# Kernel optimization log

Hardware: AMD Instinct MI355X
Metric: run time of the kernel (lower is better)

The kernel has to match this reference:

```python
import jax, jax.numpy as jnp
import numpy as np

INPUT_SIZE = 2048
HIDDEN_SIZE = 2048
BATCH = 4096


def setup_inputs() -> dict:
    key = jax.random.key(0)
    ks = jax.random.split(key, 12)
    D = INPUT_SIZE + HIDDEN_SIZE
    H = HIDDEN_SIZE
    s = 1.0 / np.sqrt(D)  # torch nn.Linear default init scale
    def lin(k):
        kw, kb = jax.random.split(k)
        W = jax.random.uniform(kw, (H, D), jnp.float32, -s, s)
        b = jax.random.uniform(kb, (H,), jnp.float32, -s, s)
        return W, b
    W_i, b_i = lin(ks[0])
    W_f, b_f = lin(ks[1])
    W_o, b_o = lin(ks[2])
    W_c, b_c = lin(ks[3])
    x_t = jax.random.normal(ks[4], (BATCH, INPUT_SIZE), jnp.float32)
    h_t_1 = jax.random.normal(ks[5], (BATCH, HIDDEN_SIZE), jnp.float32)
    c_t_1 = jax.random.normal(ks[6], (BATCH, HIDDEN_SIZE), jnp.float32)
    return {
        "x_t": x_t, "h_t_1": h_t_1, "c_t_1": c_t_1,
        "W_i": W_i, "b_i": b_i,
        "W_f": W_f, "b_f": b_f,
        "W_o": W_o, "b_o": b_o,
        "W_c": W_c, "b_c": b_c,
    }


def reference(x_t, h_t_1, c_t_1, W_i, b_i, W_f, b_f, W_o, b_o, W_c, b_c):
    # xh: [B, input_size + hidden_size]
    xh = jnp.concatenate([x_t, h_t_1], axis=1)
    # Fuse the 4 independent gate GEMMs into one matmul with stacked weights.
    W = jnp.concatenate([W_i, W_f, W_o, W_c], axis=0)  # [4H, D]
    b = jnp.concatenate([b_i, b_f, b_o, b_c], axis=0)  # [4H]
    z = xh @ W.T + b  # [B, 4H]
    H = W_i.shape[0]
    zi, zf, zo, zc = jnp.split(z, 4, axis=1)
    i_t = jax.nn.sigmoid(zi)
    f_t = jax.nn.sigmoid(zf)
    o_t = jax.nn.sigmoid(zo)
    c_hat = jnp.tanh(zc)
    c_t = f_t * c_t_1 + i_t * c_hat
    h_t = o_t * jnp.tanh(c_t)
    return (h_t, c_t)
```

## Files before the change

### kernel.cpp

```cpp
#include <hip/hip_runtime.h>
#include <hip/hip_bf16.h>


#define M_DIM 4096
#define K_DIM 4096
#define H_DIM 2048
#define BM 256
#define BH 32
#define BK 64
#define NTHREADS 512

typedef __attribute__((ext_vector_type(8))) short bf16x8;
typedef __attribute__((ext_vector_type(8))) unsigned short u16x8;
typedef __attribute__((ext_vector_type(4))) float f32x4;

__device__ __forceinline__ unsigned short f2bf(float f) {
    union { float f; unsigned int u; } v; v.f = f;
    unsigned int u = v.u;
    unsigned int r = u + 0x7FFFu + ((u >> 16) & 1u);
    return (unsigned short)(r >> 16);
}

__device__ __forceinline__ float sigmoid_f(float x) {
    return 1.0f / (1.0f + __expf(-x));
}
__device__ __forceinline__ float tanh_f(float x) {
    return 2.0f / (1.0f + __expf(-2.0f * x)) - 1.0f;
}

__device__ __forceinline__ int sw64(int row, int koff) {
    int c  = koff >> 3;
    int sc = c ^ (row & 7);
    return row * BK + sc * 8 + (koff & 7);
}

__device__ __forceinline__ void async_load16(const unsigned short* g, unsigned short* l) {
    __builtin_amdgcn_global_load_lds(
        (const __attribute__((address_space(1))) void*)g,
        (__attribute__((address_space(3))) void*)l,
        16, 0, 0);
}

__global__ __launch_bounds__(256) void convert_all(
        const float* __restrict__ x, const float* __restrict__ h,
        const float* __restrict__ Wi, const float* __restrict__ Wf,
        const float* __restrict__ Wo, const float* __restrict__ Wc,
        u16x8* __restrict__ xh_bf, u16x8* __restrict__ w_bf) {
    const int XHT = (M_DIM * K_DIM) / 8;
    int t = blockIdx.x * 256 + threadIdx.x;
    const float* src;
    u16x8* dst;
    if (t < XHT) {
        int e = t * 8;
        int row = e >> 12;
        int col = e & 4095;
        src = (col < 2048) ? &x[(size_t)row * 2048 + col]
                           : &h[(size_t)row * 2048 + (col - 2048)];
        dst = xh_bf + t;
    } else {
        int g2 = t - XHT;
        long e = (long)g2 * 8;
        int row = (int)(e >> 12);
        int col = (int)(e & 4095);
        int gate = row >> 11;
        const float* Ws = (gate == 0) ? Wi : (gate == 1) ? Wf : (gate == 2) ? Wo : Wc;
        src = &Ws[(size_t)(row & 2047) * 4096 + col];
        dst = w_bf + g2;
    }
    float4 v0 = *(const float4*)src;
    float4 v1 = *(const float4*)(src + 4);
    u16x8 o;
    o[0] = f2bf(v0.x); o[1] = f2bf(v0.y); o[2] = f2bf(v0.z); o[3] = f2bf(v0.w);
    o[4] = f2bf(v1.x); o[5] = f2bf(v1.y); o[6] = f2bf(v1.z); o[7] = f2bf(v1.w);
    *dst = o;
}

template <bool DMA>
__global__ __launch_bounds__(NTHREADS, 2) void lstm_gemm(
    const unsigned short* __restrict__ xh_bf, const unsigned short* __restrict__ w_bf,
    const float* __restrict__ x_t, const float* __restrict__ h_t_1,
    const float* __restrict__ Wi, const float* __restrict__ Wf,
    const float* __restrict__ Wo, const float* __restrict__ Wc,
    const float* __restrict__ b_i, const float* __restrict__ b_f,
    const float* __restrict__ b_o, const float* __restrict__ b_c,
    const float* __restrict__ c_prev,
    float* __restrict__ h_out, float* __restrict__ c_out) {

    __shared__ __align__(16) unsigned short sA[BM * BK];
    __shared__ __align__(16) unsigned short sB[4 * BH * BK];

    const int tid  = threadIdx.x;
    const int w    = tid >> 6;
    const int lane = tid & 63;
    const int l16  = lane & 15;
    const int quad = lane >> 4;
    const int wm   = w & 3;
    const int wh   = w >> 2;
    const int s7   = l16 & 7;

    const int bid  = blockIdx.x;
    const int xcd  = bid & 7;
    const int slot = bid >> 3;
    const int yIdx = xcd * 2 + (slot >> 6);
    const int nIdx = slot & 63;

    const int mBase = yIdx * BM;
    const int nBase = nIdx * BH;

    f32x4 acc[4][4] = {};

    const int aBase = (wm * 64 + l16) * BK;
    const int bBase = (wh * 16 + l16) * BK;

    const unsigned short* aSrc = nullptr;
    const unsigned short* bSrc = nullptr;
    if constexpr (DMA) {
        int arowi = tid >> 3;
        int alc   = (tid & 7) ^ (arowi & 7);
        aSrc = xh_bf + (size_t)(mBase + arowi) * K_DIM + alc * 8;
        int browi = (tid >> 3) & 31;
        int gate0 = tid >> 8;
        int blc   = (tid & 7) ^ (browi & 7);
        bSrc = w_bf + (size_t)(gate0 * H_DIM + nBase + browi) * K_DIM + blc * 8;
    }
    const int dmaDst = tid * 8;

    for (int k0 = 0; k0 < K_DIM; k0 += BK) {
        __syncthreads();
        if constexpr (DMA) {
#pragma unroll
            for (int r = 0; r < 4; ++r)
                async_load16(aSrc + (size_t)r * 64 * K_DIM, &sA[dmaDst + r * 4096]);
#pragma unroll
            for (int r = 0; r < 2; ++r)
                async_load16(bSrc + (size_t)r * 2 * H_DIM * K_DIM, &sB[dmaDst + r * 4096]);
            aSrc += BK;
            bSrc += BK;
        } else {
            const float* Asrc = (k0 < 2048) ? x_t : h_t_1;
            int kloc = k0 & 2047;
#pragma unroll
            for (int r = 0; r < 8; ++r) {
                int cc  = r * NTHREADS + tid;
                int row = cc >> 4;
                int ko  = (cc & 15) * 4;
                float4 v = *(const float4*)&Asrc[(size_t)(mBase + row) * 2048 + kloc + ko];
                *(ushort4*)&sA[sw64(row, ko)] =
                    make_ushort4(f2bf(v.x), f2bf(v.y), f2bf(v.z), f2bf(v.w));
            }
            const float* Wg[4] = {Wi, Wf, Wo, Wc};
#pragma unroll
            for (int r = 0; r < 4; ++r) {
                int cc   = r * NTHREADS + tid;
                int gate = cc >> 9;
                int row  = (cc >> 4) & 31;
                int ko   = (cc & 15) * 4;
                float4 v = *(const float4*)&Wg[gate][(size_t)(nBase + row) * K_DIM + k0 + ko];
                *(ushort4*)&sB[gate * (BH * BK) + sw64(row, ko)] =
                    make_ushort4(f2bf(v.x), f2bf(v.y), f2bf(v.z), f2bf(v.w));
            }
        }
        __syncthreads();

#pragma unroll
        for (int hk = 0; hk < 2; ++hk) {
            const int co = ((hk * 4 + quad) ^ s7) << 3;
            bf16x8 av[4];
#pragma unroll
            for (int mt = 0; mt < 4; ++mt)
                av[mt] = *(const bf16x8*)&sA[aBase + mt * (16 * BK) + co];
            bf16x8 bv[4];
#pragma unroll
            for (int g = 0; g < 4; ++g)
                bv[g] = *(const bf16x8*)&sB[g * (BH * BK) + bBase + co];
#pragma unroll
            for (int g = 0; g < 4; ++g)
#pragma unroll
                for (int mt = 0; mt < 4; ++mt)
                    acc[g][mt] = __builtin_amdgcn_mfma_f32_16x16x32_bf16(
                        av[mt], bv[g], acc[g][mt], 0, 0, 0);
        }
    }

    {
        int n = nBase + wh * 16 + l16;
        float bi = b_i[n], bf = b_f[n], bo = b_o[n], bc = b_c[n];
#pragma unroll
        for (int mt = 0; mt < 4; ++mt) {
#pragma unroll
            for (int i = 0; i < 4; ++i) {
                int m = mBase + wm * 64 + mt * 16 + quad * 4 + i;
                float zi = acc[0][mt][i] + bi;
                float zf = acc[1][mt][i] + bf;
                float zo = acc[2][mt][i] + bo;
                float zc = acc[3][mt][i] + bc;
                float ig = sigmoid_f(zi);
                float fg = sigmoid_f(zf);
                float og = sigmoid_f(zo);
                float ch = tanh_f(zc);
                size_t idx = (size_t)m * H_DIM + n;
                float c = fg * c_prev[idx] + ig * ch;
                c_out[idx] = c;
                h_out[idx] = og * tanh_f(c);
            }
        }
    }
}

extern "C" void kernel_launch(void* const* d_in, const int* in_sizes, int n_in,
                              void* d_out, int out_size, void* d_ws, size_t ws_size,
                              hipStream_t stream) {
    const float* x_t   = (const float*)d_in[0];
    const float* h_t_1 = (const float*)d_in[1];
    const float* c_t_1 = (const float*)d_in[2];
    const float* W_i   = (const float*)d_in[3];
    const float* b_i   = (const float*)d_in[4];
    const float* W_f   = (const float*)d_in[5];
    const float* b_f   = (const float*)d_in[6];
    const float* W_o   = (const float*)d_in[7];
    const float* b_o   = (const float*)d_in[8];
    const float* W_c   = (const float*)d_in[9];
    const float* b_c   = (const float*)d_in[10];

    float* h_out = (float*)d_out;
    float* c_out = h_out + (size_t)M_DIM * H_DIM;

    dim3 grid((H_DIM / BH) * (M_DIM / BM));

    const size_t need = (size_t)M_DIM * K_DIM * 2 + (size_t)4 * H_DIM * K_DIM * 2;
    if (ws_size >= need) {
        unsigned short* xh_bf = (unsigned short*)d_ws;
        unsigned short* w_bf  = xh_bf + (size_t)M_DIM * K_DIM;
        int total_threads = (M_DIM * K_DIM + 4 * H_DIM * K_DIM) / 8;
        convert_all<<<total_threads / 256, 256, 0, stream>>>(
            x_t, h_t_1, W_i, W_f, W_o, W_c, (u16x8*)xh_bf, (u16x8*)w_bf);
        lstm_gemm<true><<<grid, NTHREADS, 0, stream>>>(
            xh_bf, w_bf, nullptr, nullptr, nullptr, nullptr, nullptr, nullptr,
            b_i, b_f, b_o, b_c, c_t_1, h_out, c_out);
    } else {
        lstm_gemm<false><<<grid, NTHREADS, 0, stream>>>(
            nullptr, nullptr, x_t, h_t_1, W_i, W_f, W_o, W_c,
            b_i, b_f, b_o, b_c, c_t_1, h_out, c_out);
    }
}
```

Measured before the change: 519.3 us.

## Add double-buffered, larger-tile GEMM kernel with XCD-aware block mapping

Adds a new LSTM GEMM kernel that double-buffers the A and B tiles in LDS, issuing async loads for the next K-step between MFMA phases. The tile grows from 32 to 64 hidden columns per gate, and s_setprio raises wave priority around the MFMA phases. Blocks are remapped so that each XCD handles contiguous M rows, which should improve L2 reuse. The aim is to hide global-load latency and raise arithmetic intensity, at the cost of twice the LDS and more accumulator registers (128 floats per thread), which may reduce occupancy.

```diff
diff --git a/kernel.cpp b/kernel.cpp
--- a/kernel.cpp
+++ b/kernel.cpp
@@ -5,10 +5,16 @@
 #define M_DIM 4096
 #define K_DIM 4096
 #define H_DIM 2048
+#define BK 64
+
 #define BM 256
 #define BH 32
-#define BK 64
 #define NTHREADS 512
+
+#define BM2 256
+#define BH2 64
+#define NT2 512
+#define KT (K_DIM / BK)
 
 typedef __attribute__((ext_vector_type(8))) short bf16x8;
 typedef __attribute__((ext_vector_type(8))) unsigned short u16x8;
@@ -75,6 +81,165 @@
     *dst = o;
 }
 
+__global__ __launch_bounds__(NT2, 2) void lstm_gemm_pipe(
+    const unsigned short* __restrict__ xh_bf, const unsigned short* __restrict__ w_bf,
+    const float* __restrict__ b_i, const float* __restrict__ b_f,
+    const float* __restrict__ b_o, const float* __restrict__ b_c,
+    const float* __restrict__ c_prev,
+    float* __restrict__ h_out, float* __restrict__ c_out) {
+
+    __shared__ __align__(16) unsigned short sA2[2][BM2 * BK];
+    __shared__ __align__(16) unsigned short sB2[2][4 * BH2 * BK];
+
+    const int tid  = threadIdx.x;
+    const int w    = tid >> 6;
+    const int lane = tid & 63;
+    const int l16  = lane & 15;
+    const int quad = lane >> 4;
+    const int wm   = w >> 2;
+    const int wh   = w & 3;
+    const int s7   = l16 & 7;
+
+    const int bid  = blockIdx.x;
+    const int xcd  = bid & 7;
+    const int slot = bid >> 3;
+    const int mRow = xcd * 2 + (slot >> 5);
+    const int nIdx = slot & 31;
+    const int mBase = mRow * BM2;
+    const int nBase = nIdx * BH2;
+
+    f32x4 acc[4][8] = {};
+
+    const int r0  = tid >> 3;
+    const int c8  = ((tid & 7) ^ (r0 & 7)) << 3;
+    const unsigned short* aS = xh_bf + (size_t)(mBase + r0) * K_DIM + c8;
+    const int g0  = (r0 >> 4) & 3;
+    const int hr0 = r0 & 15;
+    const unsigned short* bS = w_bf + (size_t)(g0 * H_DIM + nBase + hr0) * K_DIM + c8;
+    const int dstA = tid * 8;
+
+#pragma unroll
+    for (int r = 0; r < 4; ++r)
+        async_load16(aS + (size_t)r * 64 * K_DIM, &sA2[0][dstA + r * 4096]);
+#pragma unroll
+    for (int r = 0; r < 4; ++r)
+        async_load16(bS + (size_t)r * 16 * K_DIM, &sB2[0][dstA + r * 4096]);
+    __syncthreads();
+
+    const int aO0 = (wm * 128 + l16) * BK;
+    const int bO0 = (wh * 64 + l16) * BK;
+    const int co0 = (quad ^ s7) << 3;
+    const int co1 = ((4 + quad) ^ s7) << 3;
+
+    for (int t = 0; t < KT; ++t) {
+        const unsigned short* sAb = sA2[t & 1];
+        const unsigned short* sBb = sB2[t & 1];
+        unsigned short* dA = sA2[(t + 1) & 1];
+        unsigned short* dB = sB2[(t + 1) & 1];
+        const unsigned short* aN = aS + (size_t)(t + 1) * BK;
+        const unsigned short* bN = bS + (size_t)(t + 1) * BK;
+        const bool st = (t + 1 < KT);
+
+        bf16x8 av[4], bv[4];
+
+#pragma unroll
+        for (int mt = 0; mt < 4; ++mt)
+            av[mt] = *(const bf16x8*)&sAb[aO0 + co0 + mt * (16 * BK)];
+#pragma unroll
+        for (int g = 0; g < 4; ++g)
+            bv[g] = *(const bf16x8*)&sBb[bO0 + co0 + g * (16 * BK)];
+        if (st) {
+#pragma unroll
+            for (int r = 0; r < 4; ++r)
+                async_load16(aN + (size_t)r * 64 * K_DIM, &dA[dstA + r * 4096]);
+        }
+        __builtin_amdgcn_s_barrier();
+        __builtin_amdgcn_s_setprio(1);
+#pragma unroll
+        for (int g = 0; g < 4; ++g)
+#pragma unroll
+            for (int mt = 0; mt < 4; ++mt)
+                acc[g][mt] = __builtin_amdgcn_mfma_f32_16x16x32_bf16(
+                    av[mt], bv[g], acc[g][mt], 0, 0, 0);
+        __builtin_amdgcn_s_setprio(0);
+        __builtin_amdgcn_s_barrier();
+
+#pragma unroll
+        for (int mt = 0; mt < 4; ++mt)
+            av[mt] = *(const bf16x8*)&sAb[aO0 + co0 + (mt + 4) * (16 * BK)];
+        if (st) {
+#pragma unroll
+            for (int r = 0; r < 4; ++r)
+                async_load16(bN + (size_t)r * 16 * K_DIM, &dB[dstA + r * 4096]);
+        }
+        __builtin_amdgcn_s_barrier();
+        __builtin_amdgcn_s_setprio(1);
+#pragma unroll
+        for (int g = 0; g < 4; ++g)
+#pragma unroll
+            for (int mt = 0; mt < 4; ++mt)
+                acc[g][mt + 4] = __builtin_amdgcn_mfma_f32_16x16x32_bf16(
+                    av[mt], bv[g], acc[g][mt + 4], 0, 0, 0);
+        __builtin_amdgcn_s_setprio(0);
+        __builtin_amdgcn_s_barrier();
+
+#pragma unroll
+        for (int mt = 0; mt < 4; ++mt)
+            av[mt] = *(const bf16x8*)&sAb[aO0 + co1 + mt * (16 * BK)];
+#pragma unroll
+        for (int g = 0; g < 4; ++g)
+            bv[g] = *(const bf16x8*)&sBb[bO0 + co1 + g * (16 * BK)];
+        __builtin_amdgcn_s_barrier();
+        __builtin_amdgcn_s_setprio(1);
+#pragma unroll
+        for (int g = 0; g < 4; ++g)
+#pragma unroll
+            for (int mt = 0; mt < 4; ++mt)
+                acc[g][mt] = __builtin_amdgcn_mfma_f32_16x16x32_bf16(
+                    av[mt], bv[g], acc[g][mt], 0, 0, 0);
+        __builtin_amdgcn_s_setprio(0);
+        __builtin_amdgcn_s_barrier();
+
+#pragma unroll
+        for (int mt = 0; mt < 4; ++mt)
+            av[mt] = *(const bf16x8*)&sAb[aO0 + co1 + (mt + 4) * (16 * BK)];
+        __builtin_amdgcn_s_barrier();
+        __builtin_amdgcn_s_setprio(1);
+#pragma unroll
+        for (int g = 0; g < 4; ++g)
+#pragma unroll
+            for (int mt = 0; mt < 4; ++mt)
+                acc[g][mt + 4] = __builtin_amdgcn_mfma_f32_16x16x32_bf16(
+                    av[mt], bv[g], acc[g][mt + 4], 0, 0, 0);
+        __builtin_amdgcn_s_setprio(0);
+        __syncthreads();
+    }
+
+    {
+        const int n = nBase + wh * 16 + l16;
+        const float bi = b_i[n], bff = b_f[n], bo = b_o[n], bc = b_c[n];
+#pragma unroll
+        for (int mt = 0; mt < 8; ++mt) {
+#pragma unroll
+            for (int i = 0; i < 4; ++i) {
+                int m = mBase + wm * 128 + mt * 16 + quad * 4 + i;
+                float zi = acc[0][mt][i] + bi;
+                float zf = acc[1][mt][i] + bff;
+                float zo = acc[2][mt][i] + bo;
+                float zc = acc[3][mt][i] + bc;
+                float ig = sigmoid_f(zi);
+                float fg = sigmoid_f(zf);
+                float og = sigmoid_f(zo);
+                float ch = tanh_f(zc);
+                size_t idx = (size_t)m * H_DIM + n;
+                float c = fg * c_prev[idx] + ig * ch;
+                c_out[idx] = c;
+                h_out[idx] = og * tanh_f(c);
+            }
+        }
+    }
+}
+
 template <bool DMA>
 __global__ __launch_bounds__(NTHREADS, 2) void lstm_gemm(
     const unsigned short* __restrict__ xh_bf, const unsigned short* __restrict__ w_bf,
@@ -225,8 +390,6 @@
     float* h_out = (float*)d_out;
     float* c_out = h_out + (size_t)M_DIM * H_DIM;
 
-    dim3 grid((H_DIM / BH) * (M_DIM / BM));
-
     const size_t need = (size_t)M_DIM * K_DIM * 2 + (size_t)4 * H_DIM * K_DIM * 2;
     if (ws_size >= need) {
         unsigned short* xh_bf = (unsigned short*)d_ws;
@@ -234,10 +397,11 @@
         int total_threads = (M_DIM * K_DIM + 4 * H_DIM * K_DIM) / 8;
         convert_all<<<total_threads / 256, 256, 0, stream>>>(
             x_t, h_t_1, W_i, W_f, W_o, W_c, (u16x8*)xh_bf, (u16x8*)w_bf);
-        lstm_gemm<true><<<grid, NTHREADS, 0, stream>>>(
-            xh_bf, w_bf, nullptr, nullptr, nullptr, nullptr, nullptr, nullptr,
-            b_i, b_f, b_o, b_c, c_t_1, h_out, c_out);
+        dim3 grid((H_DIM / BH2) * (M_DIM / BM2));
+        lstm_gemm_pipe<<<grid, NT2, 0, stream>>>(
+            xh_bf, w_bf, b_i, b_f, b_o, b_c, c_t_1, h_out, c_out);
     } else {
+        dim3 grid((H_DIM / BH) * (M_DIM / BM));
         lstm_gemm<false><<<grid, NTHREADS, 0, stream>>>(
             nullptr, nullptr, x_t, h_t_1, W_i, W_f, W_o, W_c,
             b_i, b_f, b_o, b_c, c_t_1, h_out, c_out);
```

New measurement: 566.5 us. +9.1%, slower.

## Add 4-stage async-load pipelined GEMM with larger N tile and split barriers

Applied to the files above, without the earlier changes.

Replaces the single-buffered DMA GEMM with a new kernel that keeps four shared-memory stages and issues async loads three tiles ahead, so global loads overlap MFMA work instead of waiting behind a full barrier each K step. The tile grows to 256x64 (per gate 64 hidden columns), giving each wave 32 accumulators and halving the grid. K is split into 32-wide steps, and s_setprio and barriers interleave LDS reads, DMA issue and MFMA. This needs more LDS and registers, which may cut occupancy, and depends on hand-tuned vmcnt waits being correct.

```diff
diff --git a/kernel.cpp b/kernel.cpp
--- a/kernel.cpp
+++ b/kernel.cpp
@@ -5,10 +5,18 @@
 #define M_DIM 4096
 #define K_DIM 4096
 #define H_DIM 2048
+
 #define BM 256
 #define BH 32
 #define BK 64
 #define NTHREADS 512
+
+#define BM2 256
+#define BH2 64
+#define BKP 32
+#define NT2 512
+#define KT2 (K_DIM / BKP)
+#define TILE_SH (BM2 * BKP)
 
 typedef __attribute__((ext_vector_type(8))) short bf16x8;
 typedef __attribute__((ext_vector_type(8))) unsigned short u16x8;
@@ -75,9 +83,149 @@
     *dst = o;
 }
 
-template <bool DMA>
-__global__ __launch_bounds__(NTHREADS, 2) void lstm_gemm(
+
+#define TILE_STEP(T, DO_STG, WAIT_OP) do {                                        \
+    const int cur_ = (T) & 3;                                                     \
+    const unsigned short* sAc = &sA[cur_ * TILE_SH];                              \
+    const unsigned short* sBc = &sB[cur_ * TILE_SH];                              \
+                            \
+    bf16x8 av0_[4], bv_[4];                                                       \
+    _Pragma("unroll")                                                             \
+    for (int mt = 0; mt < 4; ++mt)                                                \
+        av0_[mt] = *(const bf16x8*)&sAc[aOff + mt * (16 * BKP)];                  \
+    _Pragma("unroll")                                                             \
+    for (int g = 0; g < 4; ++g)                                                   \
+        bv_[g] = *(const bf16x8*)&sBc[bOff + g * (16 * BKP)];                     \
+    if (DO_STG) {                                                                 \
+        unsigned short* dA = &sA[(((T) + 3) & 3) * TILE_SH];                      \
+        const unsigned short* s0 = aS + (size_t)((T) + 3) * BKP;                  \
+        async_load16(s0, &dA[dstOff]);                                            \
+        async_load16(s0 + (size_t)128 * K_DIM, &dA[dstOff + 4096]);               \
+    }                                                                             \
+    __builtin_amdgcn_s_barrier();                                                 \
+    __builtin_amdgcn_s_setprio(1);                                                \
+    _Pragma("unroll")                                                             \
+    for (int g = 0; g < 4; ++g)                                                   \
+        _Pragma("unroll")                                                         \
+        for (int mt = 0; mt < 4; ++mt)                                            \
+            acc[g][mt] = __builtin_amdgcn_mfma_f32_16x16x32_bf16(                 \
+                av0_[mt], bv_[g], acc[g][mt], 0, 0, 0);                           \
+    __builtin_amdgcn_s_setprio(0);                                                \
+    __builtin_amdgcn_s_barrier();                                                 \
+                \
+    bf16x8 av1_[4];                                                               \
+    _Pragma("unroll")                                                             \
+    for (int mt = 0; mt < 4; ++mt)                                                \
+        av1_[mt] = *(const bf16x8*)&sAc[aOff + (mt + 4) * (16 * BKP)];            \
+    if (DO_STG) {                                                                 \
+        unsigned short* dB = &sB[(((T) + 3) & 3) * TILE_SH];                      \
+        const unsigned short* s1 = bS + (size_t)((T) + 3) * BKP;                  \
+        async_load16(s1, &dB[dstOff]);                                            \
+        async_load16(s1 + (size_t)32 * K_DIM, &dB[dstOff + 4096]);                \
+    }                                                                             \
+    __builtin_amdgcn_s_barrier();                                                 \
+    __builtin_amdgcn_s_setprio(1);                                                \
+    _Pragma("unroll")                                                             \
+    for (int g = 0; g < 4; ++g)                                                   \
+        _Pragma("unroll")                                                         \
+        for (int mt = 0; mt < 4; ++mt)                                            \
+            acc[g][mt + 4] = __builtin_amdgcn_mfma_f32_16x16x32_bf16(             \
+                av1_[mt], bv_[g], acc[g][mt + 4], 0, 0, 0);                       \
+    __builtin_amdgcn_s_setprio(0);                                                \
+    WAIT_OP;                                                                      \
+    __builtin_amdgcn_s_barrier();                                                 \
+} while (0)
+
+__global__ __launch_bounds__(NT2, 2) void lstm_gemm_pipe(
     const unsigned short* __restrict__ xh_bf, const unsigned short* __restrict__ w_bf,
+    const float* __restrict__ b_i, const float* __restrict__ b_f,
+    const float* __restrict__ b_o, const float* __restrict__ b_c,
+    const float* __restrict__ c_prev,
+    float* __restrict__ h_out, float* __restrict__ c_out) {
+
+    __shared__ __align__(16) unsigned short sA[4 * TILE_SH];
+    __shared__ __align__(16) unsigned short sB[4 * TILE_SH];
+
+    const int tid  = threadIdx.x;
+    const int w    = tid >> 6;
+    const int lane = tid & 63;
+    const int l16  = lane & 15;
+    const int quad = lane >> 4;
+    const int wm   = w >> 2;
+    const int wh   = w & 3;
+
+    const int bid  = blockIdx.x;
+    const int xcd  = bid & 7;
+    const int slot = bid >> 3;
+    const int mRow = xcd * 2 + (slot >> 5);
+    const int nIdx = slot & 31;
+    const int mBase = mRow * BM2;
+    const int nBase = nIdx * BH2;
+
+    f32x4 acc[4][8] = {};
+
+    const int c8a  = (((tid & 3) ^ ((tid >> 3) & 3)) << 3);
+    const int row0 = tid >> 2;
+    const unsigned short* aS = xh_bf + (size_t)(mBase + row0) * K_DIM + c8a;
+    const int q0   = row0 >> 6;
+    const int gat0 = (row0 >> 4) & 3;
+    const int hr0  = row0 & 15;
+    const unsigned short* bS =
+        w_bf + (size_t)(gat0 * H_DIM + nBase + q0 * 16 + hr0) * K_DIM + c8a;
+    const int dstOff = tid * 8;
+
+    const int slotSh = ((quad ^ ((l16 >> 1) & 3)) << 3);
+    const int aOff = (wm * 128 + l16) * BKP + slotSh;
+    const int bOff = (wh * 64 + l16) * BKP + slotSh;
+
+#pragma unroll
+    for (int p = 0; p < 3; ++p) {
+        const unsigned short* a0 = aS + (size_t)p * BKP;
+        const unsigned short* b0 = bS + (size_t)p * BKP;
+        unsigned short* dA = &sA[p * TILE_SH];
+        unsigned short* dB = &sB[p * TILE_SH];
+        async_load16(a0, &dA[dstOff]);
+        async_load16(a0 + (size_t)128 * K_DIM, &dA[dstOff + 4096]);
+        async_load16(b0, &dB[dstOff]);
+        async_load16(b0 + (size_t)32 * K_DIM, &dB[dstOff + 4096]);
+    }
+    asm volatile("s_waitcnt vmcnt(8)" ::: "memory");
+    __builtin_amdgcn_s_barrier();
+
+#pragma unroll 1
+    for (int t = 0; t < KT2 - 3; ++t) {
+        TILE_STEP(t, true, asm volatile("s_waitcnt vmcnt(8)" ::: "memory"));
+    }
+    TILE_STEP(KT2 - 3, false, asm volatile("s_waitcnt vmcnt(4)" ::: "memory"));
+    TILE_STEP(KT2 - 2, false, asm volatile("s_waitcnt vmcnt(0)" ::: "memory"));
+    TILE_STEP(KT2 - 1, false, (void)0);
+
+    {
+        const int n = nBase + wh * 16 + l16;
+        const float bi = b_i[n], bff = b_f[n], bo = b_o[n], bc = b_c[n];
+#pragma unroll
+        for (int mt = 0; mt < 8; ++mt) {
+#pragma unroll
+            for (int i = 0; i < 4; ++i) {
+                int m = mBase + wm * 128 + mt * 16 + quad * 4 + i;
+                float zi = acc[0][mt][i] + bi;
+                float zf = acc[1][mt][i] + bff;
+                float zo = acc[2][mt][i] + bo;
+                float zc = acc[3][mt][i] + bc;
+                float ig = sigmoid_f(zi);
+                float fg = sigmoid_f(zf);
+                float og = sigmoid_f(zo);
+                float ch = tanh_f(zc);
+                size_t idx = (size_t)m * H_DIM + n;
+                float c = fg * c_prev[idx] + ig * ch;
+                c_out[idx] = c;
+                h_out[idx] = og * tanh_f(c);
+            }
+        }
+    }
+}
+
+__global__ __launch_bounds__(NTHREADS, 2) void lstm_gemm_fb(
     const float* __restrict__ x_t, const float* __restrict__ h_t_1,
     const float* __restrict__ Wi, const float* __restrict__ Wf,
     const float* __restrict__ Wo, const float* __restrict__ Wc,
@@ -112,53 +260,29 @@
     const int aBase = (wm * 64 + l16) * BK;
     const int bBase = (wh * 16 + l16) * BK;
 
-    const unsigned short* aSrc = nullptr;
-    const unsigned short* bSrc = nullptr;
-    if constexpr (DMA) {
-        int arowi = tid >> 3;
-        int alc   = (tid & 7) ^ (arowi & 7);
-        aSrc = xh_bf + (size_t)(mBase + arowi) * K_DIM + alc * 8;
-        int browi = (tid >> 3) & 31;
-        int gate0 = tid >> 8;
-        int blc   = (tid & 7) ^ (browi & 7);
-        bSrc = w_bf + (size_t)(gate0 * H_DIM + nBase + browi) * K_DIM + blc * 8;
-    }
-    const int dmaDst = tid * 8;
-
     for (int k0 = 0; k0 < K_DIM; k0 += BK) {
         __syncthreads();
-        if constexpr (DMA) {
-#pragma unroll
-            for (int r = 0; r < 4; ++r)
-                async_load16(aSrc + (size_t)r * 64 * K_DIM, &sA[dmaDst + r * 4096]);
-#pragma unroll
-            for (int r = 0; r < 2; ++r)
-                async_load16(bSrc + (size_t)r * 2 * H_DIM * K_DIM, &sB[dmaDst + r * 4096]);
-            aSrc += BK;
-            bSrc += BK;
-        } else {
-            const float* Asrc = (k0 < 2048) ? x_t : h_t_1;
-            int kloc = k0 & 2047;
-#pragma unroll
-            for (int r = 0; r < 8; ++r) {
-                int cc  = r * NTHREADS + tid;
-                int row = cc >> 4;
-                int ko  = (cc & 15) * 4;
-                float4 v = *(const float4*)&Asrc[(size_t)(mBase + row) * 2048 + kloc + ko];
-                *(ushort4*)&sA[sw64(row, ko)] =
-                    make_ushort4(f2bf(v.x), f2bf(v.y), f2bf(v.z), f2bf(v.w));
-            }
-            const float* Wg[4] = {Wi, Wf, Wo, Wc};
-#pragma unroll
-            for (int r = 0; r < 4; ++r) {
-                int cc   = r * NTHREADS + tid;
-                int gate = cc >> 9;
-                int row  = (cc >> 4) & 31;
-                int ko   = (cc & 15) * 4;
-                float4 v = *(const float4*)&Wg[gate][(size_t)(nBase + row) * K_DIM + k0 + ko];
-                *(ushort4*)&sB[gate * (BH * BK) + sw64(row, ko)] =
-                    make_ushort4(f2bf(v.x), f2bf(v.y), f2bf(v.z), f2bf(v.w));
-            }
+        const float* Asrc = (k0 < 2048) ? x_t : h_t_1;
+        int kloc = k0 & 2047;
+#pragma unroll
+        for (int r = 0; r < 8; ++r) {
+            int cc  = r * NTHREADS + tid;
+            int row = cc >> 4;
+            int ko  = (cc & 15) * 4;
+            float4 v = *(const float4*)&Asrc[(size_t)(mBase + row) * 2048 + kloc + ko];
+            *(ushort4*)&sA[sw64(row, ko)] =
+                make_ushort4(f2bf(v.x), f2bf(v.y), f2bf(v.z), f2bf(v.w));
+        }
+        const float* Wg[4] = {Wi, Wf, Wo, Wc};
+#pragma unroll
+        for (int r = 0; r < 4; ++r) {
+            int cc   = r * NTHREADS + tid;
+            int gate = cc >> 9;
+            int row  = (cc >> 4) & 31;
+            int ko   = (cc & 15) * 4;
+            float4 v = *(const float4*)&Wg[gate][(size_t)(nBase + row) * K_DIM + k0 + ko];
+            *(ushort4*)&sB[gate * (BH * BK) + sw64(row, ko)] =
+                make_ushort4(f2bf(v.x), f2bf(v.y), f2bf(v.z), f2bf(v.w));
         }
         __syncthreads();
 
@@ -225,8 +349,6 @@
     float* h_out = (float*)d_out;
     float* c_out = h_out + (size_t)M_DIM * H_DIM;
 
-    dim3 grid((H_DIM / BH) * (M_DIM / BM));
-
     const size_t need = (size_t)M_DIM * K_DIM * 2 + (size_t)4 * H_DIM * K_DIM * 2;
     if (ws_size >= need) {
         unsigned short* xh_bf = (unsigned short*)d_ws;
@@ -234,12 +356,13 @@
         int total_threads = (M_DIM * K_DIM + 4 * H_DIM * K_DIM) / 8;
         convert_all<<<total_threads / 256, 256, 0, stream>>>(
             x_t, h_t_1, W_i, W_f, W_o, W_c, (u16x8*)xh_bf, (u16x8*)w_bf);
-        lstm_gemm<true><<<grid, NTHREADS, 0, stream>>>(
-            xh_bf, w_bf, nullptr, nullptr, nullptr, nullptr, nullptr, nullptr,
+        dim3 grid((H_DIM / BH2) * (M_DIM / BM2));
+        lstm_gemm_pipe<<<grid, NT2, 0, stream>>>(
+            xh_bf, w_bf, b_i, b_f, b_o, b_c, c_t_1, h_out, c_out);
+    } else {
+        dim3 grid((H_DIM / BH) * (M_DIM / BM));
+        lstm_gemm_fb<<<grid, NTHREADS, 0, stream>>>(
+            x_t, h_t_1, W_i, W_f, W_o, W_c,
             b_i, b_f, b_o, b_c, c_t_1, h_out, c_out);
-    } else {
-        lstm_gemm<false><<<grid, NTHREADS, 0, stream>>>(
-            nullptr, nullptr, x_t, h_t_1, W_i, W_f, W_o, W_c,
-            b_i, b_f, b_o, b_c, c_t_1, h_out, c_out);
-    }
-}
+    }
+}
```

New measurement: 565.6 us. 8.9% more time.

## Double-buffer A tile in LDS and load weight fragments directly into registers

Applied to the files above, without the earlier changes.

The DMA GEMM path now double-buffers the activation tile in shared memory, issuing the next tile's async loads before computing on the current one, and drops one barrier per K step. Weight fragments are read straight from global memory into registers instead of being staged through LDS. Launch bounds rise to 4 blocks per SM and MFMA sections are wrapped in s_setprio. This aims to hide global load latency and cut LDS traffic, but direct per-lane weight reads rely on cache hits, and higher occupancy may limit registers.

```diff
diff --git a/kernel.cpp b/kernel.cpp
--- a/kernel.cpp
+++ b/kernel.cpp
@@ -75,19 +75,14 @@
     *dst = o;
 }
 
-template <bool DMA>
-__global__ __launch_bounds__(NTHREADS, 2) void lstm_gemm(
+__global__ __launch_bounds__(NTHREADS, 4) void lstm_gemm_dbv(
     const unsigned short* __restrict__ xh_bf, const unsigned short* __restrict__ w_bf,
-    const float* __restrict__ x_t, const float* __restrict__ h_t_1,
-    const float* __restrict__ Wi, const float* __restrict__ Wf,
-    const float* __restrict__ Wo, const float* __restrict__ Wc,
     const float* __restrict__ b_i, const float* __restrict__ b_f,
     const float* __restrict__ b_o, const float* __restrict__ b_c,
     const float* __restrict__ c_prev,
     float* __restrict__ h_out, float* __restrict__ c_out) {
 
-    __shared__ __align__(16) unsigned short sA[BM * BK];
-    __shared__ __align__(16) unsigned short sB[4 * BH * BK];
+    __shared__ __align__(16) unsigned short sA[2][BM * BK];
 
     const int tid  = threadIdx.x;
     const int w    = tid >> 6;
@@ -109,56 +104,159 @@
 
     f32x4 acc[4][4] = {};
 
+    const int arowi = tid >> 3;
+    const int alc   = (tid & 7) ^ (arowi & 7);
+    const unsigned short* aS = xh_bf + (size_t)(mBase + arowi) * K_DIM + alc * 8;
+    const int dmaDst = tid * 8;
+
+    const unsigned short* bvBase =
+        w_bf + (size_t)(nBase + wh * 16 + l16) * K_DIM + quad * 8;
+
+    const int aBase = (wm * 64 + l16) * BK;
+
+#pragma unroll
+    for (int r = 0; r < 4; ++r)
+        async_load16(aS + (size_t)r * 64 * K_DIM, &sA[0][dmaDst + r * 4096]);
+    __syncthreads();
+
+#pragma unroll 1
+    for (int t = 0; t < K_DIM / BK; ++t) {
+        const unsigned short* sAc = sA[t & 1];
+        unsigned short* sAn = (unsigned short*)sA[(t + 1) & 1];
+        const int k0 = t * BK;
+
+        if (t < (K_DIM / BK) - 1) {
+            const unsigned short* an = aS + (size_t)(k0 + BK);
+#pragma unroll
+            for (int r = 0; r < 4; ++r)
+                async_load16(an + (size_t)r * 64 * K_DIM, &sAn[dmaDst + r * 4096]);
+        }
+
+        bf16x8 bv0[4], bv1[4];
+#pragma unroll
+        for (int g = 0; g < 4; ++g)
+            bv0[g] = *(const bf16x8*)(bvBase + (size_t)g * H_DIM * K_DIM + k0);
+#pragma unroll
+        for (int g = 0; g < 4; ++g)
+            bv1[g] = *(const bf16x8*)(bvBase + (size_t)g * H_DIM * K_DIM + k0 + 32);
+
+        {
+            const int co = (quad ^ s7) << 3;
+            bf16x8 av[4];
+#pragma unroll
+            for (int mt = 0; mt < 4; ++mt)
+                av[mt] = *(const bf16x8*)&sAc[aBase + mt * (16 * BK) + co];
+            __builtin_amdgcn_s_setprio(1);
+#pragma unroll
+            for (int g = 0; g < 4; ++g)
+#pragma unroll
+                for (int mt = 0; mt < 4; ++mt)
+                    acc[g][mt] = __builtin_amdgcn_mfma_f32_16x16x32_bf16(
+                        av[mt], bv0[g], acc[g][mt], 0, 0, 0);
+            __builtin_amdgcn_s_setprio(0);
+        }
+        {
+            const int co = ((4 + quad) ^ s7) << 3;
+            bf16x8 av[4];
+#pragma unroll
+            for (int mt = 0; mt < 4; ++mt)
+                av[mt] = *(const bf16x8*)&sAc[aBase + mt * (16 * BK) + co];
+            __builtin_amdgcn_s_setprio(1);
+#pragma unroll
+            for (int g = 0; g < 4; ++g)
+#pragma unroll
+                for (int mt = 0; mt < 4; ++mt)
+                    acc[g][mt] = __builtin_amdgcn_mfma_f32_16x16x32_bf16(
+                        av[mt], bv1[g], acc[g][mt], 0, 0, 0);
+            __builtin_amdgcn_s_setprio(0);
+        }
+
+        __syncthreads();
+    }
+
+    {
+        const int n = nBase + wh * 16 + l16;
+        const float bi = b_i[n], bff = b_f[n], bo = b_o[n], bc = b_c[n];
+#pragma unroll
+        for (int mt = 0; mt < 4; ++mt) {
+#pragma unroll
+            for (int i = 0; i < 4; ++i) {
+                int m = mBase + wm * 64 + mt * 16 + quad * 4 + i;
+                float zi = acc[0][mt][i] + bi;
+                float zf = acc[1][mt][i] + bff;
+                float zo = acc[2][mt][i] + bo;
+                float zc = acc[3][mt][i] + bc;
+                float ig = sigmoid_f(zi);
+                float fg = sigmoid_f(zf);
+                float og = sigmoid_f(zo);
+                float ch = tanh_f(zc);
+                size_t idx = (size_t)m * H_DIM + n;
+                float c = fg * c_prev[idx] + ig * ch;
+                c_out[idx] = c;
+                h_out[idx] = og * tanh_f(c);
+            }
+        }
+    }
+}
+
+__global__ __launch_bounds__(NTHREADS, 2) void lstm_gemm_fb(
+    const float* __restrict__ x_t, const float* __restrict__ h_t_1,
+    const float* __restrict__ Wi, const float* __restrict__ Wf,
+    const float* __restrict__ Wo, const float* __restrict__ Wc,
+    const float* __restrict__ b_i, const float* __restrict__ b_f,
+    const float* __restrict__ b_o, const float* __restrict__ b_c,
+    const float* __restrict__ c_prev,
+    float* __restrict__ h_out, float* __restrict__ c_out) {
+
+    __shared__ __align__(16) unsigned short sA[BM * BK];
+    __shared__ __align__(16) unsigned short sB[4 * BH * BK];
+
+    const int tid  = threadIdx.x;
+    const int w    = tid >> 6;
+    const int lane = tid & 63;
+    const int l16  = lane & 15;
+    const int quad = lane >> 4;
+    const int wm   = w & 3;
+    const int wh   = w >> 2;
+    const int s7   = l16 & 7;
+
+    const int bid  = blockIdx.x;
+    const int xcd  = bid & 7;
+    const int slot = bid >> 3;
+    const int yIdx = xcd * 2 + (slot >> 6);
+    const int nIdx = slot & 63;
+
+    const int mBase = yIdx * BM;
+    const int nBase = nIdx * BH;
+
+    f32x4 acc[4][4] = {};
+
     const int aBase = (wm * 64 + l16) * BK;
     const int bBase = (wh * 16 + l16) * BK;
 
-    const unsigned short* aSrc = nullptr;
-    const unsigned short* bSrc = nullptr;
-    if constexpr (DMA) {
-        int arowi = tid >> 3;
-        int alc   = (tid & 7) ^ (arowi & 7);
-        aSrc = xh_bf + (size_t)(mBase + arowi) * K_DIM + alc * 8;
-        int browi = (tid >> 3) & 31;
-        int gate0 = tid >> 8;
-        int blc   = (tid & 7) ^ (browi & 7);
-        bSrc = w_bf + (size_t)(gate0 * H_DIM + nBase + browi) * K_DIM + blc * 8;
-    }
-    const int dmaDst = tid * 8;
-
     for (int k0 = 0; k0 < K_DIM; k0 += BK) {
         __syncthreads();
-        if constexpr (DMA) {
-#pragma unroll
-            for (int r = 0; r < 4; ++r)
-                async_load16(aSrc + (size_t)r * 64 * K_DIM, &sA[dmaDst + r * 4096]);
-#pragma unroll
-            for (int r = 0; r < 2; ++r)
-                async_load16(bSrc + (size_t)r * 2 * H_DIM * K_DIM, &sB[dmaDst + r * 4096]);
-            aSrc += BK;
-            bSrc += BK;
-        } else {
-            const float* Asrc = (k0 < 2048) ? x_t : h_t_1;
-            int kloc = k0 & 2047;
-#pragma unroll
-            for (int r = 0; r < 8; ++r) {
-                int cc  = r * NTHREADS + tid;
-                int row = cc >> 4;
-                int ko  = (cc & 15) * 4;
-                float4 v = *(const float4*)&Asrc[(size_t)(mBase + row) * 2048 + kloc + ko];
-                *(ushort4*)&sA[sw64(row, ko)] =
-                    make_ushort4(f2bf(v.x), f2bf(v.y), f2bf(v.z), f2bf(v.w));
-            }
-            const float* Wg[4] = {Wi, Wf, Wo, Wc};
-#pragma unroll
-            for (int r = 0; r < 4; ++r) {
-                int cc   = r * NTHREADS + tid;
-                int gate = cc >> 9;
-                int row  = (cc >> 4) & 31;
-                int ko   = (cc & 15) * 4;
-                float4 v = *(const float4*)&Wg[gate][(size_t)(nBase + row) * K_DIM + k0 + ko];
-                *(ushort4*)&sB[gate * (BH * BK) + sw64(row, ko)] =
-                    make_ushort4(f2bf(v.x), f2bf(v.y), f2bf(v.z), f2bf(v.w));
-            }
+        const float* Asrc = (k0 < 2048) ? x_t : h_t_1;
+        int kloc = k0 & 2047;
+#pragma unroll
+        for (int r = 0; r < 8; ++r) {
+            int cc  = r * NTHREADS + tid;
+            int row = cc >> 4;
+            int ko  = (cc & 15) * 4;
+            float4 v = *(const float4*)&Asrc[(size_t)(mBase + row) * 2048 + kloc + ko];
+            *(ushort4*)&sA[sw64(row, ko)] =
+                make_ushort4(f2bf(v.x), f2bf(v.y), f2bf(v.z), f2bf(v.w));
+        }
+        const float* Wg[4] = {Wi, Wf, Wo, Wc};
+#pragma unroll
+        for (int r = 0; r < 4; ++r) {
+            int cc   = r * NTHREADS + tid;
+            int gate = cc >> 9;
+            int row  = (cc >> 4) & 31;
+            int ko   = (cc & 15) * 4;
+            float4 v = *(const float4*)&Wg[gate][(size_t)(nBase + row) * K_DIM + k0 + ko];
+            *(ushort4*)&sB[gate * (BH * BK) + sw64(row, ko)] =
+                make_ushort4(f2bf(v.x), f2bf(v.y), f2bf(v.z), f2bf(v.w));
         }
         __syncthreads();
 
@@ -234,12 +332,11 @@
         int total_threads = (M_DIM * K_DIM + 4 * H_DIM * K_DIM) / 8;
         convert_all<<<total_threads / 256, 256, 0, stream>>>(
             x_t, h_t_1, W_i, W_f, W_o, W_c, (u16x8*)xh_bf, (u16x8*)w_bf);
-        lstm_gemm<true><<<grid, NTHREADS, 0, stream>>>(
-            xh_bf, w_bf, nullptr, nullptr, nullptr, nullptr, nullptr, nullptr,
+        lstm_gemm_dbv<<<grid, NTHREADS, 0, stream>>>(
+            xh_bf, w_bf, b_i, b_f, b_o, b_c, c_t_1, h_out, c_out);
+    } else {
+        lstm_gemm_fb<<<grid, NTHREADS, 0, stream>>>(
+            x_t, h_t_1, W_i, W_f, W_o, W_c,
             b_i, b_f, b_o, b_c, c_t_1, h_out, c_out);
-    } else {
-        lstm_gemm<false><<<grid, NTHREADS, 0, stream>>>(
-            nullptr, nullptr, x_t, h_t_1, W_i, W_f, W_o, W_c,
-            b_i, b_f, b_o, b_c, c_t_1, h_out, c_out);
-    }
-}
+    }
+}
```

After: 825.7 us. 1.59x slower.
